# Kernel tuning notes

Measured on AMD Instinct MI355X. Metric: run time of the kernel, lower is better.

The kernel has to match this reference:

```python
import jax, jax.numpy as jnp
import numpy as np

M, N = 8192, 8192
BITS = 3
BETA1, BETA2 = 16, 16
NNZ_PER_ROW = 32


def setup_inputs() -> dict:
    key = jax.random.key(0)
    ks = jax.random.split(key, 10)
    tm, tn = M // BETA1, N // BETA2
    nnz = M * NNZ_PER_ROW
    x = jax.random.normal(ks[0], (1, 10, N), dtype=jnp.float32)
    # quantized weight codes and first-order quantized scale/zero codes (3-bit)
    W = jax.random.randint(ks[1], (M, N), 0, 2 ** BITS, dtype=jnp.int32)
    W_s = jax.random.randint(ks[2], (M, tn), 0, 2 ** BITS, dtype=jnp.int32)
    W_z = jax.random.randint(ks[3], (M, tn), 0, 2 ** BITS, dtype=jnp.int32)
    # second-order (per-tile) float scale/zero for the quantized scales/zeros
    W_s_s = jax.random.uniform(ks[4], (tm, tn), jnp.float32, 0.01, 0.1)
    W_s_z = jax.random.uniform(ks[5], (tm, tn), jnp.float32, 0.0, 1.0)
    W_z_s = jax.random.uniform(ks[6], (tm, tn), jnp.float32, 0.01, 0.1)
    W_z_z = jax.random.uniform(ks[7], (tm, tn), jnp.float32, 0.0, 1.0)
    # CSR outliers: fixed 32 nnz per row
    row_offsets = jnp.arange(M + 1, dtype=jnp.int32) * NNZ_PER_ROW
    col_ids = jax.random.randint(ks[8], (nnz,), 0, N, dtype=jnp.int32)
    values = jax.random.normal(ks[9], (nnz,), dtype=jnp.float32)
    return dict(x=x, W=W, W_s=W_s, W_z=W_z, W_s_s=W_s_s, W_s_z=W_s_z,
                W_z_s=W_z_s, W_z_z=W_z_z, row_offsets=row_offsets,
                col_ids=col_ids, values=values)


def _dequantize(W, W_s, W_z, W_s_s, W_s_z, W_z_s, W_z_z):
    m, n = W.shape
    tm, tn = W_s_s.shape
    beta1, beta2 = m // tm, n // tn
    # two-level dequant: first-order scale/zero are themselves quantized per tile
    s = (W_s.astype(jnp.float32).reshape(tm, beta1, tn) - W_s_z[:, None, :]) * W_s_s[:, None, :]
    z = (W_z.astype(jnp.float32).reshape(tm, beta1, tn) - W_z_z[:, None, :]) * W_z_s[:, None, :]
    s = s.reshape(m, tn)  # (m, n/beta2)
    z = z.reshape(m, tn)
    w = (W.astype(jnp.float32).reshape(m, tn, beta2) - z[:, :, None]) * s[:, :, None]
    return w.reshape(m, n)


def reference(x, W, W_s, W_z, W_s_s, W_s_z, W_z_s, W_z_z, row_offsets, col_ids, values):
    Wd = _dequantize(W, W_s, W_z, W_s_s, W_s_z, W_z_s, W_z_z)  # (m, n)
    m = Wd.shape[0]
    b, l, n = x.shape
    xf = x.reshape(b * l, n)
    # dense quantized matmul: y = x @ Wd^T
    y = jnp.einsum('bn,mn->bm', xf, Wd)
    # CSR sparse outlier correction
    nnz = values.shape[0]
    rows = jnp.repeat(jnp.arange(m, dtype=jnp.int32), jnp.diff(row_offsets),
                      total_repeat_length=nnz)
    contrib = values[:, None] * xf[:, col_ids].T  # (nnz, B)
    y = y + jax.ops.segment_sum(contrib, rows, num_segments=m).T
    return y.reshape(b, l, m)
```

## Files before the change

### kernel.cpp

```cpp
#include <hip/hip_runtime.h>
#include <hip/hip_bf16.h>


constexpr int M_DIM = 8192;
constexpr int N_DIM = 8192;
constexpr int TN    = 512;
constexpr int BQ    = 10;
constexpr int KSPLIT = 16;
constexpr int KRANGE = N_DIM / KSPLIT;
constexpr int KITERS = KRANGE / 32;
constexpr int RPB    = 64;
constexpr int GPB    = KRANGE / 16;
constexpr int DEPTH  = 6;

typedef float  f32x4  __attribute__((ext_vector_type(4)));
typedef int    i32x4  __attribute__((ext_vector_type(4)));
typedef short  bf16x8 __attribute__((ext_vector_type(8)));

__device__ inline int pkbf(float a, float b) {
    __hip_bfloat162 h = __float22bfloat162_rn(float2{a, b});
    int r;
    __builtin_memcpy(&r, &h, 4);
    return r;
}

__global__ __launch_bounds__(256, 4)
void spqr_mfma(const float* __restrict__ x,
               const int*   __restrict__ W,
               const int*   __restrict__ Ws,
               const int*   __restrict__ Wz,
               const float* __restrict__ Wss,
               const float* __restrict__ Wsz,
               const float* __restrict__ Wzs,
               const float* __restrict__ Wzz,
               const int*   __restrict__ row_offsets,
               const int*   __restrict__ col_ids,
               const float* __restrict__ values,
               float*       __restrict__ pws)
{
    const int t   = threadIdx.x;
    const int m0b = blockIdx.x * RPB;
    const int ks  = blockIdx.y;

    if (ks == KSPLIT) {
        const int r8 = t >> 5;
        const int j  = t & 31;
        float* pb = pws + (size_t)KSPLIT * (BQ * N_DIM);
        for (int rr = r8; rr < RPB; rr += 8) {
            const int m = m0b + rr;
            const int base = row_offsets[m];
            const int cnt  = row_offsets[m + 1] - base;
            float c[BQ];
            #pragma unroll
            for (int b = 0; b < BQ; ++b) c[b] = 0.f;
            for (int jj = j; jj < cnt; jj += 32) {
                const int   col = col_ids[base + jj];
                const float v   = values[base + jj];
                #pragma unroll
                for (int b = 0; b < BQ; ++b)
                    c[b] = fmaf(v, x[b * N_DIM + col], c[b]);
            }
            #pragma unroll
            for (int b = 0; b < BQ; ++b) {
                float v = c[b];
                for (int off = 16; off > 0; off >>= 1)
                    v += __shfl_xor(v, off, 32);
                c[b] = v;
            }
            if (j == 0) {
                #pragma unroll
                for (int b = 0; b < BQ; ++b)
                    pb[(size_t)b * N_DIM + m] = c[b];
            }
        }
        return;
    }

    __shared__ int ldsA[KITERS * 64 * 4];
    __shared__ int ldsSZ[RPB * 33];

    const int k0 = ks * KRANGE;
    const int g0 = k0 >> 4;

    for (int idx = t; idx < KITERS * 64; idx += 256) {
        const int kk = idx >> 6, l = idx & 63;
        const int b = l & 15, koff = (kk << 5) + ((l >> 4) << 3);
        int out[4] = {0, 0, 0, 0};
        if (b < BQ) {
            const float* xp = x + b * N_DIM + k0 + koff;
            f32x4 lo = *reinterpret_cast<const f32x4*>(xp);
            f32x4 hi = *reinterpret_cast<const f32x4*>(xp + 4);
            out[0] = pkbf(lo.x, lo.y);
            out[1] = pkbf(lo.z, lo.w);
            out[2] = pkbf(hi.x, hi.y);
            out[3] = pkbf(hi.z, hi.w);
        }
        *reinterpret_cast<i32x4*>(&ldsA[idx * 4]) = *reinterpret_cast<i32x4*>(out);
    }

    for (int idx = t; idx < RPB * GPB; idx += 256) {
        const int rl = idx >> 5;
        const int gl = idx & 31;
        const int m = m0b + rl, g = g0 + gl;
        const int tix = (m >> 4) * TN + g;
        const float s = ((float)Ws[m * TN + g] - Wsz[tix]) * Wss[tix];
        const float z = ((float)Wz[m * TN + g] - Wzz[tix]) * Wzs[tix];
        ldsSZ[rl * 33 + gl] = pkbf(s, -z * s);
    }
    __syncthreads();

    const int wv = t >> 6, l = t & 63;
    const int lrow = l & 15;
    const int lk   = l >> 4;
    const int m0   = m0b + (wv << 4);
    const int* wp  = W + (size_t)(m0 + lrow) * N_DIM + k0 + (lk << 3);
    const int szrow = (wv << 4) + lrow;
    const int szk   = lk >> 1;

    f32x4 acc = {0.f, 0.f, 0.f, 0.f};
    i32x4 cbufL[DEPTH], cbufH[DEPTH];

    #pragma unroll
    for (int p = 0; p < DEPTH; ++p) {
        cbufL[p] = *reinterpret_cast<const i32x4*>(wp + p * 32);
        cbufH[p] = *reinterpret_cast<const i32x4*>(wp + p * 32 + 4);
    }

    #pragma unroll
    for (int kk = 0; kk < KITERS; ++kk) {
        const i32x4 cl = cbufL[kk % DEPTH], ch = cbufH[kk % DEPTH];
        if (kk + DEPTH < KITERS) {
            cbufL[kk % DEPTH] =
                *reinterpret_cast<const i32x4*>(wp + (kk + DEPTH) * 32);
            cbufH[kk % DEPTH] =
                *reinterpret_cast<const i32x4*>(wp + (kk + DEPTH) * 32 + 4);
        }
        const i32x4 a4 = *reinterpret_cast<const i32x4*>(&ldsA[(kk * 64 + l) * 4]);
        const int spk = ldsSZ[szrow * 33 + kk * 2 + szk];
        const float s   = __uint_as_float((unsigned)spk << 16);
        const float nzs = __uint_as_float((unsigned)spk & 0xffff0000u);
        int bw[4];
        bw[0] = pkbf(fmaf((float)cl.x, s, nzs), fmaf((float)cl.y, s, nzs));
        bw[1] = pkbf(fmaf((float)cl.z, s, nzs), fmaf((float)cl.w, s, nzs));
        bw[2] = pkbf(fmaf((float)ch.x, s, nzs), fmaf((float)ch.y, s, nzs));
        bw[3] = pkbf(fmaf((float)ch.z, s, nzs), fmaf((float)ch.w, s, nzs));
        const bf16x8 af = __builtin_bit_cast(bf16x8, a4);
        i32x4 bwv = *reinterpret_cast<i32x4*>(bw);
        const bf16x8 bf = __builtin_bit_cast(bf16x8, bwv);
        acc = __builtin_amdgcn_mfma_f32_16x16x32_bf16(af, bf, acc, 0, 0, 0);
    }

    float* pb = pws + (size_t)ks * (BQ * N_DIM) + (m0 + lrow);
    #pragma unroll
    for (int j = 0; j < 4; ++j) {
        const int b = (lk << 2) + j;
        if (b < BQ) pb[(size_t)b * N_DIM] = acc[j];
    }
}

__global__ __launch_bounds__(256, 4)
void spqr_reduce(const float* __restrict__ pws,
                 float*       __restrict__ y)
{
    const int gid = blockIdx.x * 256 + threadIdx.x;
    if (gid >= BQ * M_DIM) return;
    const int b = gid / M_DIM;
    const int m = gid - b * M_DIM;
    const float* pp = pws + (size_t)b * N_DIM + m;
    float v = 0.f;
    #pragma unroll
    for (int ksp = 0; ksp < KSPLIT + 1; ++ksp)
        v += pp[(size_t)ksp * (BQ * N_DIM)];
    y[(size_t)b * M_DIM + m] = v;
}

extern "C" void kernel_launch(void* const* d_in, const int* in_sizes, int n_in,
                              void* d_out, int out_size, void* d_ws, size_t ws_size,
                              hipStream_t stream)
{
    const float* x    = (const float*)d_in[0];
    const int*   W    = (const int*)  d_in[1];
    const int*   Ws   = (const int*)  d_in[2];
    const int*   Wz   = (const int*)  d_in[3];
    const float* Wss  = (const float*)d_in[4];
    const float* Wsz  = (const float*)d_in[5];
    const float* Wzs  = (const float*)d_in[6];
    const float* Wzz  = (const float*)d_in[7];
    const int*   roff = (const int*)  d_in[8];
    const int*   cids = (const int*)  d_in[9];
    const float* vals = (const float*)d_in[10];
    float* yout = (float*)d_out;
    float* pws  = (float*)d_ws;

    dim3 grid1(M_DIM / RPB, KSPLIT + 1);
    spqr_mfma<<<grid1, dim3(256), 0, stream>>>(x, W, Ws, Wz, Wss, Wsz, Wzs, Wzz,
                                               roff, cids, vals, pws);

    dim3 grid2((BQ * M_DIM + 255) / 256);
    spqr_reduce<<<grid2, dim3(256), 0, stream>>>(pws, yout);
}
```

Measured before the change: 82.77 us.

## Stream weight codes via direct-to-LDS async loads with XOR-swizzled double buffer

Replaces the six-deep register prefetch of the int32 weight codes with per-wave global_load_lds copies into a two-stage LDS buffer, using an XOR swizzle on the staging layout and on the scale/zero table to avoid bank conflicts. The aim is to cut VGPR pressure and let the memory system fill LDS asynchronously while dequant and MFMA run. In exchange, only one stage is now in flight ahead of compute, so fewer bytes are outstanding per wave on a bandwidth-bound stream. LDS use per block also grows, which may limit occupancy.

```diff
diff --git a/kernel.cpp b/kernel.cpp
--- a/kernel.cpp
+++ b/kernel.cpp
@@ -11,17 +11,25 @@
 constexpr int KITERS = KRANGE / 32;
 constexpr int RPB    = 64;
 constexpr int GPB    = KRANGE / 16;
-constexpr int DEPTH  = 6;
 
 typedef float  f32x4  __attribute__((ext_vector_type(4)));
 typedef int    i32x4  __attribute__((ext_vector_type(4)));
 typedef short  bf16x8 __attribute__((ext_vector_type(8)));
+
+#define AS1C(p) ((const __attribute__((address_space(1))) void*)(p))
+#define AS3(p)  ((__attribute__((address_space(3))) void*)(p))
 
 __device__ inline int pkbf(float a, float b) {
     __hip_bfloat162 h = __float22bfloat162_rn(float2{a, b});
     int r;
     __builtin_memcpy(&r, &h, 4);
     return r;
+}
+
+template<int N>
+__device__ __forceinline__ void wait_vm() {
+    asm volatile("s_waitcnt vmcnt(%0)" :: "n"(N));
+    __builtin_amdgcn_sched_barrier(0);
 }
 
 __global__ __launch_bounds__(256, 4)
@@ -77,14 +85,36 @@
     }
 
     __shared__ int ldsA[KITERS * 64 * 4];
-    __shared__ int ldsSZ[RPB * 33];
+    __shared__ int ldsSZ[RPB * 32];
+    __shared__ int stg[2 * 4 * 512];
 
     const int k0 = ks * KRANGE;
     const int g0 = k0 >> 4;
 
+    const int wv = t >> 6, l = t & 63;
+    const int lrow = l & 15;
+    const int lk   = l >> 4;
+    const int m0   = m0b + (wv << 4);
+
+    const int sr0 = l >> 3;
+    const int sc0 = (l & 7) ^ (sr0 & 7);
+    const int sr1 = sr0 + 8;
+    const int sc1 = (l & 7) ^ (sr1 & 7);
+    const int* gs0 = W + (size_t)(m0 + sr0) * N_DIM + k0 + sc0 * 4;
+    const int* gs1 = W + (size_t)(m0 + sr1) * N_DIM + k0 + sc1 * 4;
+    int* stw = &stg[wv * 512];
+
+#define STAGE(kk) do {                                                        \
+    int* d_ = stw + ((kk) & 1) * 2048;                                        \
+    __builtin_amdgcn_global_load_lds(AS1C(gs0 + (kk) * 32), AS3(d_),       16, 0, 0); \
+    __builtin_amdgcn_global_load_lds(AS1C(gs1 + (kk) * 32), AS3(d_ + 256), 16, 0, 0); \
+} while (0)
+
+    STAGE(0);
+
     for (int idx = t; idx < KITERS * 64; idx += 256) {
-        const int kk = idx >> 6, l = idx & 63;
-        const int b = l & 15, koff = (kk << 5) + ((l >> 4) << 3);
+        const int kk = idx >> 6, ll = idx & 63;
+        const int b = ll & 15, koff = (kk << 5) + ((ll >> 4) << 3);
         int out[4] = {0, 0, 0, 0};
         if (b < BQ) {
             const float* xp = x + b * N_DIM + k0 + koff;
@@ -105,38 +135,26 @@
         const int tix = (m >> 4) * TN + g;
         const float s = ((float)Ws[m * TN + g] - Wsz[tix]) * Wss[tix];
         const float z = ((float)Wz[m * TN + g] - Wzz[tix]) * Wzs[tix];
-        ldsSZ[rl * 33 + gl] = pkbf(s, -z * s);
+        ldsSZ[rl * 32 + (gl ^ (rl & 31))] = pkbf(s, -z * s);
     }
     __syncthreads();
 
-    const int wv = t >> 6, l = t & 63;
-    const int lrow = l & 15;
-    const int lk   = l >> 4;
-    const int m0   = m0b + (wv << 4);
-    const int* wp  = W + (size_t)(m0 + lrow) * N_DIM + k0 + (lk << 3);
     const int szrow = (wv << 4) + lrow;
     const int szk   = lk >> 1;
+    const int roff  = lrow * 32 + (((lk * 2) ^ (lrow & 7)) * 4);
 
     f32x4 acc = {0.f, 0.f, 0.f, 0.f};
-    i32x4 cbufL[DEPTH], cbufH[DEPTH];
-
-    #pragma unroll
-    for (int p = 0; p < DEPTH; ++p) {
-        cbufL[p] = *reinterpret_cast<const i32x4*>(wp + p * 32);
-        cbufH[p] = *reinterpret_cast<const i32x4*>(wp + p * 32 + 4);
-    }
 
     #pragma unroll
     for (int kk = 0; kk < KITERS; ++kk) {
-        const i32x4 cl = cbufL[kk % DEPTH], ch = cbufH[kk % DEPTH];
-        if (kk + DEPTH < KITERS) {
-            cbufL[kk % DEPTH] =
-                *reinterpret_cast<const i32x4*>(wp + (kk + DEPTH) * 32);
-            cbufH[kk % DEPTH] =
-                *reinterpret_cast<const i32x4*>(wp + (kk + DEPTH) * 32 + 4);
-        }
+        if (kk + 1 < KITERS) STAGE(kk + 1);
         const i32x4 a4 = *reinterpret_cast<const i32x4*>(&ldsA[(kk * 64 + l) * 4]);
-        const int spk = ldsSZ[szrow * 33 + kk * 2 + szk];
+        const int gi  = kk * 2 + szk;
+        const int spk = ldsSZ[szrow * 32 + (gi ^ (szrow & 31))];
+        if (kk + 1 < KITERS) wait_vm<2>(); else wait_vm<0>();
+        const int* tile = stw + (kk & 1) * 2048;
+        const i32x4 cl = *reinterpret_cast<const i32x4*>(&tile[roff]);
+        const i32x4 ch = *reinterpret_cast<const i32x4*>(&tile[roff ^ 4]);
         const float s   = __uint_as_float((unsigned)spk << 16);
         const float nzs = __uint_as_float((unsigned)spk & 0xffff0000u);
         int bw[4];
@@ -149,6 +167,7 @@
         const bf16x8 bf = __builtin_bit_cast(bf16x8, bwv);
         acc = __builtin_amdgcn_mfma_f32_16x16x32_bf16(af, bf, acc, 0, 0, 0);
     }
+#undef STAGE
 
     float* pb = pws + (size_t)ks * (BQ * N_DIM) + (m0 + lrow);
     #pragma unroll
```

Result: slower. 107.1 us (+29.4%).
